# Performance work log

Measured on AMD Instinct MI355X. Metric: run time of the kernel, lower is better.

Reference implementation:

```python
import jax, jax.numpy as jnp
import numpy as np

B, N, D_IN, D_OUT, H = 4, 2048, 1024, 1024, 16
HD = D_OUT // H

def _xavier(key, shape):
    fan_in, fan_out = shape[0], shape[1]
    a = jnp.sqrt(6.0 / (fan_in + fan_out))
    return jax.random.uniform(key, shape, jnp.float32, -a, a)

def setup_inputs() -> dict:
    key = jax.random.key(0)
    ks = jax.random.split(key, 6)
    x = jax.random.normal(ks[0], (B, N, D_IN), jnp.float32)
    w_q = _xavier(ks[1], (D_IN, D_OUT))
    w_k = _xavier(ks[2], (D_IN, D_OUT))
    w_v = _xavier(ks[3], (D_IN, D_OUT))
    # nn.Linear default init: uniform(-1/sqrt(fan_in), 1/sqrt(fan_in))
    bound = 1.0 / jnp.sqrt(D_OUT)
    w_o = jax.random.uniform(ks[4], (D_OUT, D_OUT), jnp.float32, -bound, bound)
    b_o = jax.random.uniform(ks[5], (D_OUT,), jnp.float32, -bound, bound)
    return {"x": x, "w_q": w_q, "w_k": w_k, "w_v": w_v, "w_o": w_o, "b_o": b_o}

def reference(x, w_q, w_k, w_v, w_o, b_o):
    b, n, _ = x.shape
    def split_heads(t):  # [b,n,D_OUT] -> [b,H,n,HD]
        return t.reshape(b, n, H, HD).transpose(0, 2, 1, 3)
    q = split_heads(x @ w_q)
    k = split_heads(x @ w_k)
    v = split_heads(x @ w_v)
    scores = jnp.einsum('bhqd,bhkd->bhqk', q, k) / jnp.sqrt(jnp.float32(HD))
    attn = jax.nn.softmax(scores, axis=-1)
    out = jnp.einsum('bhqk,bhkd->bhqd', attn, v)
    out = out.transpose(0, 2, 1, 3).reshape(b, n, D_OUT)
    return out @ w_o + b_o
```

## Files before the change

### kernel.cpp

```cpp
#include <hip/hip_runtime.h>
#include <stdint.h>
#include <stddef.h>

typedef __attribute__((ext_vector_type(8))) short bf16x8_t;
typedef __attribute__((ext_vector_type(4))) float f32x4_t;
typedef __attribute__((ext_vector_type(16))) float f32x16_t;
typedef __attribute__((ext_vector_type(4))) unsigned int u32x4_t;
typedef __attribute__((ext_vector_type(2))) unsigned int u32x2_t;

__device__ __forceinline__ unsigned short f2bf(float f) {
  union { float f; unsigned int u; } x; x.f = f;
  unsigned int r = x.u + 0x7fffu + ((x.u >> 16) & 1u);
  return (unsigned short)(r >> 16);
}

__device__ __forceinline__ float e2(float x) { return __builtin_amdgcn_exp2f(x); }

__device__ __forceinline__ unsigned int cvtpk(float lo, float hi) {
  unsigned int d;
  asm("v_cvt_pk_bf16_f32 %0, %1, %2" : "=v"(d) : "v"(lo), "v"(hi));
  return d;
}
__device__ __forceinline__ void plswap(unsigned int& a, unsigned int& b) {
  asm("v_permlane32_swap_b32 %0, %1" : "+v"(a), "+v"(b));
}

__device__ __forceinline__ void gload16(const void* g, void* l) {
  __builtin_amdgcn_global_load_lds(
      (const __attribute__((address_space(1))) void*)g,
      (__attribute__((address_space(3))) void*)l, 16, 0, 0);
}

#define QSCALE 0.18033688011112042f

__global__ __launch_bounds__(256)
void f32_to_bf16(const float* __restrict__ in, unsigned short* __restrict__ out) {
  size_t i = ((size_t)blockIdx.x * 256 + threadIdx.x) * 8;
  f32x4_t a = *(const f32x4_t*)(in + i);
  f32x4_t b = *(const f32x4_t*)(in + i + 4);
  bf16x8_t o;
#pragma unroll
  for (int j = 0; j < 4; ++j) { o[j] = (short)f2bf(a[j]); o[j + 4] = (short)f2bf(b[j]); }
  *(bf16x8_t*)(out + i) = o;
}

__global__ __launch_bounds__(256)
void transpose_cvt3(const float* __restrict__ w0, const float* __restrict__ w1,
                    const float* __restrict__ w2, unsigned short* __restrict__ out) {
  __shared__ float t[32][33];
  const float* in = blockIdx.z == 0 ? w0 : (blockIdx.z == 1 ? w1 : w2);
  unsigned short* o = out + (size_t)blockIdx.z * 1024 * 1024;
  const int x = threadIdx.x & 31, y = threadIdx.x >> 5;
  const int bx = blockIdx.x * 32, by = blockIdx.y * 32;
#pragma unroll
  for (int i = 0; i < 32; i += 8)
    t[y + i][x] = in[(size_t)(by + y + i) * 1024 + bx + x];
  __syncthreads();
#pragma unroll
  for (int i = 0; i < 32; i += 8)
    o[(size_t)(bx + y + i) * 1024 + by + x] = f2bf(t[x][y + i]);
}

__global__ __launch_bounds__(256)
void transpose_cvt(const float* __restrict__ in, unsigned short* __restrict__ out) {
  __shared__ float t[32][33];
  const int x = threadIdx.x & 31, y = threadIdx.x >> 5;
  const int bx = blockIdx.x * 32, by = blockIdx.y * 32;
#pragma unroll
  for (int i = 0; i < 32; i += 8)
    t[y + i][x] = in[(size_t)(by + y + i) * 1024 + bx + x];
  __syncthreads();
#pragma unroll
  for (int i = 0; i < 32; i += 8)
    out[(size_t)(bx + y + i) * 1024 + by + x] = f2bf(t[x][y + i]);
}

__global__ __launch_bounds__(256)
void transpose_v(const unsigned short* __restrict__ in, unsigned short* __restrict__ out) {
  __shared__ unsigned short t[64][65];
  const int bh = blockIdx.y;
  const int n0 = blockIdx.x * 64;
  const int c = threadIdx.x & 63, r4 = threadIdx.x >> 6;
#pragma unroll
  for (int i = 0; i < 64; i += 4)
    t[r4 + i][c] = in[((size_t)bh * 2048 + n0 + r4 + i) * 64 + c];
  __syncthreads();
#pragma unroll
  for (int i = 0; i < 64; i += 4)
    out[((size_t)bh * 64 + r4 + i) * 2048 + n0 + c] = t[c][r4 + i];
}

template <int MODE>
__global__ __launch_bounds__(256, 3)
void gemm128(const unsigned short* __restrict__ A,
             const unsigned short* __restrict__ Bt,
             void* __restrict__ Cv,
             const float* __restrict__ bias,
             int M, int K, int Nn) {
  constexpr int BK = 32;
  __shared__ __align__(16) unsigned short As[2][128 * BK];
  __shared__ __align__(16) unsigned short Bs[2][128 * BK];

  const int tid = threadIdx.x;
  const int wave = tid >> 6;
  const int lane = tid & 63;
  const int l15 = lane & 15;
  const int lq = lane >> 4;

  const int bid = blockIdx.x;
  const int xcd = bid & 7, tt = bid >> 3;
  const int row0 = (xcd * 8 + (tt & 7)) * 128;
  const int col0 = (tt >> 3) * 128;

  const int wr = (wave >> 1) * 64;
  const int wc = (wave & 1) * 64;

  f32x4_t acc[4][4];
#pragma unroll
  for (int m = 0; m < 4; ++m)
#pragma unroll
    for (int n = 0; n < 4; ++n) acc[m][n] = (f32x4_t)0.f;

  const int p0 = tid, p1 = tid + 256;
  const int pr0 = p0 >> 2, ps0 = (p0 & 3) ^ (pr0 & 3);
  const int pr1 = p1 >> 2, ps1 = (p1 & 3) ^ (pr1 & 3);

  const unsigned short* Ap0 = A + (size_t)(row0 + pr0) * K + ps0 * 8;
  const unsigned short* Ap1 = A + (size_t)(row0 + pr1) * K + ps1 * 8;
  const unsigned short* Bp0 = Bt + (size_t)(col0 + pr0) * K + ps0 * 8;
  const unsigned short* Bp1 = Bt + (size_t)(col0 + pr1) * K + ps1 * 8;

  {
    char* ab = (char*)As[0];
    char* bb = (char*)Bs[0];
    gload16(Ap0, ab + p0 * 16);
    gload16(Ap1, ab + p1 * 16);
    gload16(Bp0, bb + p0 * 16);
    gload16(Bp1, bb + p1 * 16);
  }
  __syncthreads();

  const int NIT = K / BK;
  for (int it = 0; it < NIT; ++it) {
    const int cur = it & 1;
    if (it + 1 < NIT) {
      const int k0n = (it + 1) * BK;
      char* ab = (char*)As[cur ^ 1];
      char* bb = (char*)Bs[cur ^ 1];
      gload16(Ap0 + k0n, ab + p0 * 16);
      gload16(Ap1 + k0n, ab + p1 * 16);
      gload16(Bp0 + k0n, bb + p0 * 16);
      gload16(Bp1 + k0n, bb + p1 * 16);
    }

    const char* Ac = (const char*)As[cur];
    const char* Bc = (const char*)Bs[cur];
    bf16x8_t af[4], bfr[4];
#pragma unroll
    for (int m = 0; m < 4; ++m) {
      int r = wr + m * 16 + l15;
      af[m] = *(const bf16x8_t*)(Ac + r * 64 + ((lq ^ (r & 3)) << 4));
    }
#pragma unroll
    for (int n = 0; n < 4; ++n) {
      int c = wc + n * 16 + l15;
      bfr[n] = *(const bf16x8_t*)(Bc + c * 64 + ((lq ^ (c & 3)) << 4));
    }
#pragma unroll
    for (int m = 0; m < 4; ++m)
#pragma unroll
      for (int n = 0; n < 4; ++n)
        acc[m][n] = __builtin_amdgcn_mfma_f32_16x16x32_bf16(af[m], bfr[n], acc[m][n], 0, 0, 0);

    __syncthreads();
  }

#pragma unroll
  for (int m = 0; m < 4; ++m) {
    int rb = row0 + wr + m * 16 + lq * 4;
#pragma unroll
    for (int n = 0; n < 4; ++n) {
      int col = col0 + wc + n * 16 + l15;
#pragma unroll
      for (int j = 0; j < 4; ++j) {
        int row = rb + j;
        float v = acc[m][n][j];
        if constexpr (MODE == 0) {
          int which = col >> 10, cl = col & 1023;
          int b = row >> 11, nn = row & 2047, h = cl >> 6, hd = cl & 63;
          float s = (which == 0) ? QSCALE : 1.0f;
          ((unsigned short*)Cv)[(size_t)which * 8388608 +
                                (((size_t)(b * 16 + h)) * 2048 + nn) * 64 + hd] = f2bf(v * s);
        } else {
          ((float*)Cv)[(size_t)row * Nn + col] = v + bias[col];
        }
      }
    }
  }
}

__global__ __launch_bounds__(512, 4)
void attn_mfma(const unsigned short* __restrict__ qb,
               const unsigned short* __restrict__ kb,
               const unsigned short* __restrict__ vtb,
               unsigned short* __restrict__ ab) {
  __shared__ __align__(16) unsigned short Ks[2][8192];
  __shared__ __align__(16) unsigned short Vs[2][8192];

  const int tid = threadIdx.x, wave = tid >> 6, lane = tid & 63;
  const int l31 = lane & 31, hi = lane >> 5;

  const int bid = blockIdx.x;
  const int xcd = bid & 7, w = bid >> 3;
  const int bh = xcd * 8 + (w >> 3);
  const int q0 = (w & 7) * 256;

  const unsigned short* qrow = qb + ((size_t)bh * 2048 + q0 + wave * 32 + l31) * 64;
  bf16x8_t qf[4];
#pragma unroll
  for (int ks = 0; ks < 4; ++ks)
    qf[ks] = *(const bf16x8_t*)(qrow + ks * 16 + hi * 8);

  f32x16_t O[2];
#pragma unroll
  for (int hb = 0; hb < 2; ++hb) O[hb] = (f32x16_t)0.f;
  float m_run = -1e30f, l_run = 0.f;

  const unsigned short* kbase = kb + (size_t)bh * 2048 * 64;
  const unsigned short* vbase = vtb + (size_t)bh * 64 * 2048;
  int koff[2], voff[2];
#pragma unroll
  for (int i = 0; i < 2; ++i) {
    int c = tid + 512 * i;
    int kr = c >> 3, kp = c & 7, kl = kp ^ (kr & 7);
    koff[i] = kr * 64 + kl * 8;
    int vr = c >> 4, vp = c & 15, vl = (vp & 8) | ((vp & 7) ^ (vr & 7));
    voff[i] = vr * 2048 + vl * 8;
  }

#pragma unroll
  for (int i = 0; i < 2; ++i) {
    gload16(kbase + koff[i], (char*)Ks[0] + (tid + 512 * i) * 16);
    gload16(vbase + voff[i], (char*)Vs[0] + (tid + 512 * i) * 16);
  }
  __syncthreads();

  for (int t = 0; t < 16; ++t) {
    const int cur = t & 1;
    if (t < 15) {
      const unsigned short* kt = kbase + (size_t)(t + 1) * 8192;
      const unsigned short* vt = vbase + (t + 1) * 128;
#pragma unroll
      for (int i = 0; i < 2; ++i) {
        gload16(kt + koff[i], (char*)Ks[cur ^ 1] + (tid + 512 * i) * 16);
        gload16(vt + voff[i], (char*)Vs[cur ^ 1] + (tid + 512 * i) * 16);
      }
    }
    const char* Kc = (const char*)Ks[cur];
    const char* Vc = (const char*)Vs[cur];

    f32x16_t sacc[4];
#pragma unroll
    for (int kbk = 0; kbk < 4; ++kbk) sacc[kbk] = (f32x16_t)0.f;
#pragma unroll
    for (int kbk = 0; kbk < 4; ++kbk) {
#pragma unroll
      for (int ks = 0; ks < 4; ++ks) {
        int key = kbk * 32 + l31;
        bf16x8_t kf = *(const bf16x8_t*)(Kc + key * 128 + (((ks * 2 + hi) ^ (key & 7)) << 4));
        sacc[kbk] = __builtin_amdgcn_mfma_f32_32x32x16_bf16(kf, qf[ks], sacc[kbk], 0, 0, 0);
      }
    }

    float mx = -1e30f;
#pragma unroll
    for (int kbk = 0; kbk < 4; ++kbk)
#pragma unroll
      for (int r = 0; r < 16; ++r) mx = fmaxf(mx, sacc[kbk][r]);
    mx = fmaxf(mx, __shfl_xor(mx, 32));

    const float mn = fmaxf(m_run, mx);
    const float alpha = e2(m_run - mn);
    m_run = mn;
    l_run *= alpha;
#pragma unroll
    for (int hb = 0; hb < 2; ++hb)
#pragma unroll
      for (int r = 0; r < 16; ++r) O[hb][r] *= alpha;

    float psum = 0.f;
#pragma unroll
    for (int kbk = 0; kbk < 4; ++kbk) {
      float p[16];
#pragma unroll
      for (int r = 0; r < 16; ++r) {
        p[r] = e2(sacc[kbk][r] - m_run);
        psum += p[r];
      }
#pragma unroll
      for (int u = 0; u < 2; ++u) {
        unsigned int a0 = cvtpk(p[8 * u + 0], p[8 * u + 1]);
        unsigned int b0 = cvtpk(p[8 * u + 4], p[8 * u + 5]);
        plswap(a0, b0);
        unsigned int a1 = cvtpk(p[8 * u + 2], p[8 * u + 3]);
        unsigned int b1 = cvtpk(p[8 * u + 6], p[8 * u + 7]);
        plswap(a1, b1);
        u32x4_t fw; fw[0] = a0; fw[1] = a1; fw[2] = b0; fw[3] = b1;
        bf16x8_t pfrag = *(bf16x8_t*)&fw;
        const int ks2 = kbk * 2 + u;
#pragma unroll
        for (int hb = 0; hb < 2; ++hb) {
          int hd = hb * 32 + l31;
          int sl = ks2 * 2 + hi;
          bf16x8_t vf = *(const bf16x8_t*)(Vc + hd * 256 +
                          (((sl & 8) | ((sl & 7) ^ (hd & 7))) << 4));
          O[hb] = __builtin_amdgcn_mfma_f32_32x32x16_bf16(vf, pfrag, O[hb], 0, 0, 0);
        }
      }
    }
    psum += __shfl_xor(psum, 32);
    l_run += psum;

    __syncthreads();
  }

  const int b = bh >> 4, h = bh & 15;
  const float inv = 1.f / l_run;
  const int row = q0 + wave * 32 + l31;
  unsigned short* op = ab + ((size_t)(b * 2048 + row)) * 1024 + h * 64;
#pragma unroll
  for (int hb = 0; hb < 2; ++hb)
#pragma unroll
    for (int tt = 0; tt < 4; ++tt) {
      u32x2_t d;
      d[0] = cvtpk(O[hb][4 * tt + 0] * inv, O[hb][4 * tt + 1] * inv);
      d[1] = cvtpk(O[hb][4 * tt + 2] * inv, O[hb][4 * tt + 3] * inv);
      *(u32x2_t*)(op + hb * 32 + tt * 8 + hi * 4) = d;
    }
}

extern "C" void kernel_launch(void* const* d_in, const int* in_sizes, int n_in,
                              void* d_out, int out_size, void* d_ws, size_t ws_size,
                              hipStream_t stream) {
  const float* x  = (const float*)d_in[0];
  const float* wq = (const float*)d_in[1];
  const float* wk = (const float*)d_in[2];
  const float* wv = (const float*)d_in[3];
  const float* wo = (const float*)d_in[4];
  const float* bo = (const float*)d_in[5];
  float* out = (float*)d_out;

  const size_t MB = 1ull << 20;
  char* ws = (char*)d_ws;
  unsigned short* xb  = (unsigned short*)(ws);
  unsigned short* ab  = xb;
  unsigned short* qkv = (unsigned short*)(ws + 17 * MB);
  unsigned short* vtb = (unsigned short*)(ws + 68 * MB);
  unsigned short* wT  = (unsigned short*)(ws + 85 * MB);
  unsigned short* woT = (unsigned short*)(ws + 91 * MB);

  const size_t X = 8388608;

  const dim3 tb(256);
  f32_to_bf16<<<4096, tb, 0, stream>>>(x, xb);
  transpose_cvt3<<<dim3(32, 32, 3), tb, 0, stream>>>(wq, wk, wv, wT);
  transpose_cvt<<<dim3(32, 32), tb, 0, stream>>>(wo, woT);

  gemm128<0><<<dim3(1536), tb, 0, stream>>>(xb, wT, (void*)qkv, nullptr, 8192, 1024, 3072);

  transpose_v<<<dim3(32, 64), tb, 0, stream>>>(qkv + 2 * X, vtb);

  attn_mfma<<<dim3(512), dim3(512), 0, stream>>>(qkv, qkv + X, vtb, ab);

  gemm128<1><<<dim3(512), tb, 0, stream>>>(ab, woT, (void*)out, bo, 8192, 1024, 1024);
}
```

Measured before the change: 291.8 us.

## Enlarge GEMM tiles to 256x128 with 8 waves, add setprio around MFMAs

The projection GEMMs move from 128x128 tiles with 4 waves to 256x128 tiles with 8 waves, so each B tile is shared across twice as many rows and fewer blocks are launched. The XCD-aware block mapping gains a rowTiles parameter. In both the GEMM and the attention kernel, s_setprio raises wave priority around the MFMA bursts, and the softmax max and sum reductions become trees to shorten dependency chains. The larger tiles use more LDS per block and lower the block count, which can reduce occupancy and leave CUs underfilled in the output GEMM.

```diff
diff --git a/kernel.cpp b/kernel.cpp
--- a/kernel.cpp
+++ b/kernel.cpp
@@ -91,15 +91,14 @@
 }
 
 template <int MODE>
-__global__ __launch_bounds__(256, 3)
-void gemm128(const unsigned short* __restrict__ A,
+__global__ __launch_bounds__(512, 4)
+void gemm256(const unsigned short* __restrict__ A,
              const unsigned short* __restrict__ Bt,
              void* __restrict__ Cv,
              const float* __restrict__ bias,
-             int M, int K, int Nn) {
-  constexpr int BK = 32;
-  __shared__ __align__(16) unsigned short As[2][128 * BK];
-  __shared__ __align__(16) unsigned short Bs[2][128 * BK];
+             int M, int K, int Nn, int rowTiles) {
+  __shared__ __align__(16) unsigned short As[2][256 * 32];
+  __shared__ __align__(16) unsigned short Bs[2][128 * 32];
 
   const int tid = threadIdx.x;
   const int wave = tid >> 6;
@@ -108,9 +107,9 @@
   const int lq = lane >> 4;
 
   const int bid = blockIdx.x;
-  const int xcd = bid & 7, tt = bid >> 3;
-  const int row0 = (xcd * 8 + (tt & 7)) * 128;
-  const int col0 = (tt >> 3) * 128;
+  const int xcd = bid & 7, tb = bid >> 3;
+  const int row0 = (xcd * rowTiles + (tb % rowTiles)) * 256;
+  const int col0 = (tb / rowTiles) * 128;
 
   const int wr = (wave >> 1) * 64;
   const int wc = (wave & 1) * 64;
@@ -121,36 +120,28 @@
 #pragma unroll
     for (int n = 0; n < 4; ++n) acc[m][n] = (f32x4_t)0.f;
 
-  const int p0 = tid, p1 = tid + 256;
-  const int pr0 = p0 >> 2, ps0 = (p0 & 3) ^ (pr0 & 3);
-  const int pr1 = p1 >> 2, ps1 = (p1 & 3) ^ (pr1 & 3);
-
-  const unsigned short* Ap0 = A + (size_t)(row0 + pr0) * K + ps0 * 8;
-  const unsigned short* Ap1 = A + (size_t)(row0 + pr1) * K + ps1 * 8;
-  const unsigned short* Bp0 = Bt + (size_t)(col0 + pr0) * K + ps0 * 8;
-  const unsigned short* Bp1 = Bt + (size_t)(col0 + pr1) * K + ps1 * 8;
-
-  {
-    char* ab = (char*)As[0];
-    char* bb = (char*)Bs[0];
-    gload16(Ap0, ab + p0 * 16);
-    gload16(Ap1, ab + p1 * 16);
-    gload16(Bp0, bb + p0 * 16);
-    gload16(Bp1, bb + p1 * 16);
-  }
-  __syncthreads();
-
-  const int NIT = K / BK;
+  const int pa0 = tid, pa1 = tid + 512, pb = tid;
+  const int ra0 = pa0 >> 2, sa0 = (pa0 & 3) ^ (ra0 & 3);
+  const int ra1 = pa1 >> 2, sa1 = (pa1 & 3) ^ (ra1 & 3);
+  const int rb  = pb >> 2,  sb  = (pb & 3) ^ (rb & 3);
+
+  const unsigned short* Ap0 = A + (size_t)(row0 + ra0) * K + sa0 * 8;
+  const unsigned short* Ap1 = A + (size_t)(row0 + ra1) * K + sa1 * 8;
+  const unsigned short* Bp0 = Bt + (size_t)(col0 + rb) * K + sb * 8;
+
+  gload16(Ap0, (char*)As[0] + pa0 * 16);
+  gload16(Ap1, (char*)As[0] + pa1 * 16);
+  gload16(Bp0, (char*)Bs[0] + pb * 16);
+  __syncthreads();
+
+  const int NIT = K / 32;
   for (int it = 0; it < NIT; ++it) {
     const int cur = it & 1;
     if (it + 1 < NIT) {
-      const int k0n = (it + 1) * BK;
-      char* ab = (char*)As[cur ^ 1];
-      char* bb = (char*)Bs[cur ^ 1];
-      gload16(Ap0 + k0n, ab + p0 * 16);
-      gload16(Ap1 + k0n, ab + p1 * 16);
-      gload16(Bp0 + k0n, bb + p0 * 16);
-      gload16(Bp1 + k0n, bb + p1 * 16);
+      const int k0n = (it + 1) * 32;
+      gload16(Ap0 + k0n, (char*)As[cur ^ 1] + pa0 * 16);
+      gload16(Ap1 + k0n, (char*)As[cur ^ 1] + pa1 * 16);
+      gload16(Bp0 + k0n, (char*)Bs[cur ^ 1] + pb * 16);
     }
 
     const char* Ac = (const char*)As[cur];
@@ -166,24 +157,26 @@
       int c = wc + n * 16 + l15;
       bfr[n] = *(const bf16x8_t*)(Bc + c * 64 + ((lq ^ (c & 3)) << 4));
     }
+    __builtin_amdgcn_s_setprio(1);
 #pragma unroll
     for (int m = 0; m < 4; ++m)
 #pragma unroll
       for (int n = 0; n < 4; ++n)
         acc[m][n] = __builtin_amdgcn_mfma_f32_16x16x32_bf16(af[m], bfr[n], acc[m][n], 0, 0, 0);
+    __builtin_amdgcn_s_setprio(0);
 
     __syncthreads();
   }
 
 #pragma unroll
   for (int m = 0; m < 4; ++m) {
-    int rb = row0 + wr + m * 16 + lq * 4;
+    int rbase = row0 + wr + m * 16 + lq * 4;
 #pragma unroll
     for (int n = 0; n < 4; ++n) {
       int col = col0 + wc + n * 16 + l15;
 #pragma unroll
       for (int j = 0; j < 4; ++j) {
-        int row = rb + j;
+        int row = rbase + j;
         float v = acc[m][n][j];
         if constexpr (MODE == 0) {
           int which = col >> 10, cl = col & 1023;
@@ -262,6 +255,7 @@
     f32x16_t sacc[4];
 #pragma unroll
     for (int kbk = 0; kbk < 4; ++kbk) sacc[kbk] = (f32x16_t)0.f;
+    __builtin_amdgcn_s_setprio(1);
 #pragma unroll
     for (int kbk = 0; kbk < 4; ++kbk) {
 #pragma unroll
@@ -271,12 +265,23 @@
         sacc[kbk] = __builtin_amdgcn_mfma_f32_32x32x16_bf16(kf, qf[ks], sacc[kbk], 0, 0, 0);
       }
     }
-
-    float mx = -1e30f;
-#pragma unroll
-    for (int kbk = 0; kbk < 4; ++kbk)
-#pragma unroll
-      for (int r = 0; r < 16; ++r) mx = fmaxf(mx, sacc[kbk][r]);
+    __builtin_amdgcn_s_setprio(0);
+
+    float mk[4];
+#pragma unroll
+    for (int kbk = 0; kbk < 4; ++kbk) {
+      float a0 = fmaxf(sacc[kbk][0], sacc[kbk][8]);
+      float a1 = fmaxf(sacc[kbk][1], sacc[kbk][9]);
+      float a2 = fmaxf(sacc[kbk][2], sacc[kbk][10]);
+      float a3 = fmaxf(sacc[kbk][3], sacc[kbk][11]);
+      float a4 = fmaxf(sacc[kbk][4], sacc[kbk][12]);
+      float a5 = fmaxf(sacc[kbk][5], sacc[kbk][13]);
+      float a6 = fmaxf(sacc[kbk][6], sacc[kbk][14]);
+      float a7 = fmaxf(sacc[kbk][7], sacc[kbk][15]);
+      a0 = fmaxf(a0, a4); a1 = fmaxf(a1, a5); a2 = fmaxf(a2, a6); a3 = fmaxf(a3, a7);
+      mk[kbk] = fmaxf(fmaxf(a0, a1), fmaxf(a2, a3));
+    }
+    float mx = fmaxf(fmaxf(mk[0], mk[1]), fmaxf(mk[2], mk[3]));
     mx = fmaxf(mx, __shfl_xor(mx, 32));
 
     const float mn = fmaxf(m_run, mx);
@@ -293,10 +298,11 @@
     for (int kbk = 0; kbk < 4; ++kbk) {
       float p[16];
 #pragma unroll
-      for (int r = 0; r < 16; ++r) {
-        p[r] = e2(sacc[kbk][r] - m_run);
-        psum += p[r];
-      }
+      for (int r = 0; r < 16; ++r) p[r] = e2(sacc[kbk][r] - mn);
+      float s0 = p[0] + p[8],  s1 = p[1] + p[9],  s2 = p[2] + p[10], s3 = p[3] + p[11];
+      float s4 = p[4] + p[12], s5 = p[5] + p[13], s6 = p[6] + p[14], s7 = p[7] + p[15];
+      s0 += s4; s1 += s5; s2 += s6; s3 += s7;
+      psum += (s0 + s1) + (s2 + s3);
 #pragma unroll
       for (int u = 0; u < 2; ++u) {
         unsigned int a0 = cvtpk(p[8 * u + 0], p[8 * u + 1]);
@@ -308,6 +314,7 @@
         u32x4_t fw; fw[0] = a0; fw[1] = a1; fw[2] = b0; fw[3] = b1;
         bf16x8_t pfrag = *(bf16x8_t*)&fw;
         const int ks2 = kbk * 2 + u;
+        __builtin_amdgcn_s_setprio(1);
 #pragma unroll
         for (int hb = 0; hb < 2; ++hb) {
           int hd = hb * 32 + l31;
@@ -316,6 +323,7 @@
                           (((sl & 8) | ((sl & 7) ^ (hd & 7))) << 4));
           O[hb] = __builtin_amdgcn_mfma_f32_32x32x16_bf16(vf, pfrag, O[hb], 0, 0, 0);
         }
+        __builtin_amdgcn_s_setprio(0);
       }
     }
     psum += __shfl_xor(psum, 32);
@@ -366,11 +374,13 @@
   transpose_cvt3<<<dim3(32, 32, 3), tb, 0, stream>>>(wq, wk, wv, wT);
   transpose_cvt<<<dim3(32, 32), tb, 0, stream>>>(wo, woT);
 
-  gemm128<0><<<dim3(1536), tb, 0, stream>>>(xb, wT, (void*)qkv, nullptr, 8192, 1024, 3072);
+  gemm256<0><<<dim3(768), dim3(512), 0, stream>>>(xb, wT, (void*)qkv, nullptr,
+                                                  8192, 1024, 3072, 4);
 
   transpose_v<<<dim3(32, 64), tb, 0, stream>>>(qkv + 2 * X, vtb);
 
   attn_mfma<<<dim3(512), dim3(512), 0, stream>>>(qkv, qkv + X, vtb, ab);
 
-  gemm128<1><<<dim3(512), tb, 0, stream>>>(ab, woT, (void*)out, bo, 8192, 1024, 1024);
-}
+  gemm256<1><<<dim3(256), dim3(512), 0, stream>>>(ab, woT, (void*)out, bo,
+                                                  8192, 1024, 1024, 4);
+}
```

New measurement: 309.5 us. 6.1% more time.
